# Kernel optimization log

Hardware: AMD Instinct MI355X
Metric: run time of the kernel (lower is better)

## Reference

```python
import jax, jax.numpy as jnp
import numpy as np

NEG_SLOPE = 0.2
EPS = 1e-6


def setup_inputs() -> dict:
    key = jax.random.key(0)
    k1, k2 = jax.random.split(key)
    B, C, N = 4, 64, 32768
    x = jax.random.normal(k1, (B, C, 3, N), dtype=jnp.float32)
    # VNLinear weight: nn.Linear(in, out, bias=False).weight -> [out, in]
    W = jax.random.normal(k2, (C, C), dtype=jnp.float32) * (1.0 / np.sqrt(C))
    return {"x": x, "W": W}


def reference(x, W):
    # VNLinear: kron(W, eye(3)) conv2d == per-3-vector channel mix
    # d[b,o,v,n] = sum_i W[o,i] * x[b,i,v,n]
    d = jnp.einsum('oi,bivn->bovn', W, x)
    dotprod = jnp.sum(x * d, axis=2, keepdims=True)      # [B,C,1,N]
    d_norm_sq = jnp.sum(d * d, axis=2, keepdims=True)    # [B,C,1,N]
    neg = x - (1.0 - NEG_SLOPE) * (dotprod / (d_norm_sq + EPS)) * d
    return jnp.where(dotprod >= 0, x, neg)
```

## Files before the change

### kernel.cpp

```cpp
#include <hip/hip_runtime.h>

#define NEG_SLOPE 0.2f
#define EPS 1e-6f


#define C_CH 64
#define V_DIM 3
#define N_FULL 32768
#define NT 32
#define THREADS 256

typedef __attribute__((ext_vector_type(8))) short bf16x8;
typedef __attribute__((ext_vector_type(4))) float f32x4;

__device__ __forceinline__ ushort f2bf(float f) {
    union { float f; unsigned u; } v; v.f = f;
    unsigned r = v.u + 0x7FFFu + ((v.u >> 16) & 1u);
    return (ushort)(r >> 16);
}
__device__ __forceinline__ float bf2f(ushort s) {
    union { unsigned u; float f; } v; v.u = ((unsigned)s) << 16; return v.f;
}
__device__ __forceinline__ unsigned pack_hl(float x) {
    union { float f; unsigned u; } a; a.f = x;
    unsigned uh = (a.u + 0x8000u) & 0xffff0000u;
    union { unsigned u; float f; } hb; hb.u = uh;
    union { float f; unsigned u; } rb; rb.f = x - hb.f;
    return uh | (rb.u >> 16);
}
__device__ __forceinline__ float u2f(unsigned u) {
    union { unsigned u; float f; } v; v.u = u; return v.f;
}

__global__ void w_split_kernel(const float* __restrict__ W,
                               ushort* __restrict__ whi, ushort* __restrict__ wlo) {
    int i = blockIdx.x * 256 + threadIdx.x;
    if (i < C_CH * C_CH) {
        float w = W[i];
        ushort h = f2bf(w);
        whi[i] = h;
        wlo[i] = f2bf(w - bf2f(h));
    }
}

template<bool USE_WS>
__global__ __launch_bounds__(THREADS, 6)
void vn_mfma32(const float* __restrict__ x,
               const float* __restrict__ Wf,
               const ushort* __restrict__ whi, const ushort* __restrict__ wlo,
               float* __restrict__ out) {
    __shared__ unsigned xs[V_DIM * C_CH][NT];

    const int t    = threadIdx.x;
    const int tile = blockIdx.x;
    const int b    = tile >> 10;
    const int n0   = (tile & 1023) << 5;

    const float* xb = x + (size_t)b * (C_CH * V_DIM * N_FULL) + n0;

    const int lane = t & 63;
    const int w    = t >> 6;
    const int wo   = w >> 1;
    const int wn   = w & 1;
    const int l4   = lane & 15;
    const int hi   = lane >> 4;

    bf16x8 Ah[2][2], Al[2][2];
    if (USE_WS) {
        #pragma unroll
        for (int m = 0; m < 2; ++m)
            #pragma unroll
            for (int kh = 0; kh < 2; ++kh) {
                size_t off = (size_t)(wo * 32 + m * 16 + l4) * C_CH + kh * 32 + hi * 8;
                Ah[m][kh] = *(const bf16x8*)(whi + off);
                Al[m][kh] = *(const bf16x8*)(wlo + off);
            }
    } else {
        #pragma unroll
        for (int m = 0; m < 2; ++m)
            #pragma unroll
            for (int kh = 0; kh < 2; ++kh) {
                const float* wp = Wf + (size_t)(wo * 32 + m * 16 + l4) * C_CH + kh * 32 + hi * 8;
                float4 wa = *(const float4*)wp;
                float4 wb = *(const float4*)(wp + 4);
                float wf[8] = {wa.x, wa.y, wa.z, wa.w, wb.x, wb.y, wb.z, wb.w};
                bf16x8 h, l;
                #pragma unroll
                for (int j = 0; j < 8; ++j) {
                    ushort hb = f2bf(wf[j]);
                    h[j] = (short)hb;
                    l[j] = (short)f2bf(wf[j] - bf2f(hb));
                }
                Ah[m][kh] = h; Al[m][kh] = l;
            }
    }

    #pragma unroll
    for (int it = 0; it < 6; ++it) {
        int idx = t + it * THREADS;
        int r   = idx >> 3;
        int c4  = (idx & 7) << 2;
        int i   = (r * 171) >> 9;
        int v   = r - 3 * i;
        int rowp = v * 64 + i;
        float4 vf4 = *(const float4*)(xb + (size_t)r * N_FULL + c4);
        float vf[4] = {vf4.x, vf4.y, vf4.z, vf4.w};
        unsigned p[4];
        #pragma unroll
        for (int q = 0; q < 4; ++q) p[q] = pack_hl(vf[q]);
        int col = c4 ^ (((rowp >> 3) & 1) << 4);
        *(uint4*)&xs[rowp][col] = *(const uint4*)p;
    }
    __syncthreads();

    f32x4 acc[2][3];
    #pragma unroll
    for (int m = 0; m < 2; ++m)
        #pragma unroll
        for (int v = 0; v < 3; ++v)
            acc[m][v] = (f32x4){0.f, 0.f, 0.f, 0.f};

    const int bcol = (wn * 16 + l4) ^ ((hi & 1) << 4);
    #pragma unroll
    for (int v = 0; v < 3; ++v) {
        #pragma unroll
        for (int kh = 0; kh < 2; ++kh) {
            unsigned p[8];
            #pragma unroll
            for (int j = 0; j < 8; ++j)
                p[j] = xs[v * 64 + kh * 32 + hi * 8 + j][bcol];
            union { bf16x8 v8; unsigned d[4]; } BH, BL;
            #pragma unroll
            for (int q = 0; q < 4; ++q) {
                BH.d[q] = __builtin_amdgcn_perm(p[2 * q + 1], p[2 * q], 0x07060302u);
                BL.d[q] = __builtin_amdgcn_perm(p[2 * q + 1], p[2 * q], 0x05040100u);
            }
            #pragma unroll
            for (int m = 0; m < 2; ++m) {
                acc[m][v] = __builtin_amdgcn_mfma_f32_16x16x32_bf16(Ah[m][kh], BH.v8, acc[m][v], 0, 0, 0);
                acc[m][v] = __builtin_amdgcn_mfma_f32_16x16x32_bf16(Ah[m][kh], BL.v8, acc[m][v], 0, 0, 0);
                acc[m][v] = __builtin_amdgcn_mfma_f32_16x16x32_bf16(Al[m][kh], BH.v8, acc[m][v], 0, 0, 0);
            }
        }
    }

    const int n    = wn * 16 + l4;
    const int ecol = n ^ ((hi >> 1) << 4);
    float* ob = out + (size_t)b * (C_CH * V_DIM * N_FULL) + n0 + n;
    #pragma unroll
    for (int m = 0; m < 2; ++m) {
        #pragma unroll
        for (int r = 0; r < 4; ++r) {
            const int o = wo * 32 + m * 16 + hi * 4 + r;
            float xv[3], dv[3];
            #pragma unroll
            for (int v = 0; v < 3; ++v) {
                unsigned p = xs[v * 64 + o][ecol];
                xv[v] = u2f(p & 0xffff0000u) + u2f(p << 16);
                dv[v] = acc[m][v][r];
            }
            float dot  = xv[0] * dv[0] + xv[1] * dv[1] + xv[2] * dv[2];
            float dnsq = dv[0] * dv[0] + dv[1] * dv[1] + dv[2] * dv[2];
            float f = (1.0f - NEG_SLOPE) * dot / (dnsq + EPS);
            float o0, o1, o2;
            if (dot >= 0.f) {
                o0 = xv[0]; o1 = xv[1]; o2 = xv[2];
            } else {
                o0 = xv[0] - f * dv[0]; o1 = xv[1] - f * dv[1]; o2 = xv[2] - f * dv[2];
            }
            float* op = ob + (size_t)o * (V_DIM * N_FULL);
            op[0 * N_FULL] = o0;
            op[1 * N_FULL] = o1;
            op[2 * N_FULL] = o2;
        }
    }
}

extern "C" void kernel_launch(void* const* d_in, const int* in_sizes, int n_in,
                              void* d_out, int out_size, void* d_ws, size_t ws_size,
                              hipStream_t stream) {
    const float* x = (const float*)d_in[0];
    const float* W = (const float*)d_in[1];
    float* out = (float*)d_out;

    const int B = 4;
    const int blocks = B * (N_FULL / NT);

    if (ws_size >= 2u * C_CH * C_CH * sizeof(ushort)) {
        ushort* whi = (ushort*)d_ws;
        ushort* wlo = whi + C_CH * C_CH;
        w_split_kernel<<<(C_CH * C_CH + 255) / 256, 256, 0, stream>>>(W, whi, wlo);
        vn_mfma32<true><<<blocks, THREADS, 0, stream>>>(x, W, whi, wlo, out);
    } else {
        vn_mfma32<false><<<blocks, THREADS, 0, stream>>>(x, W, nullptr, nullptr, out);
    }
}
```

Baseline: 44.74 us.

## Swap MFMA operands so each lane owns 4 contiguous n for float4 stores

Swaps the A/B operands of the MFMA so x becomes the A operand and W the B operand. Each lane's accumulator then holds 4 consecutive n positions for one output channel instead of 4 channels at one n. The epilogue can read x from LDS as uint4 and write the output as float4, where it used to do scalar loads and stores. The LDS swizzle is extended to keep the new access patterns free of bank conflicts. The change also replaces the division with a fast reciprocal, which slightly alters rounding.

```diff
diff --git a/kernel.cpp b/kernel.cpp
--- a/kernel.cpp
+++ b/kernel.cpp
@@ -23,10 +23,10 @@
 }
 __device__ __forceinline__ unsigned pack_hl(float x) {
     union { float f; unsigned u; } a; a.f = x;
-    unsigned uh = (a.u + 0x8000u) & 0xffff0000u;
-    union { unsigned u; float f; } hb; hb.u = uh;
+    unsigned t0 = a.u + 0x8000u;
+    union { unsigned u; float f; } hb; hb.u = t0 & 0xffff0000u;
     union { float f; unsigned u; } rb; rb.f = x - hb.f;
-    return uh | (rb.u >> 16);
+    return __builtin_amdgcn_perm(t0, rb.u, 0x07060302u);
 }
 __device__ __forceinline__ float u2f(unsigned u) {
     union { unsigned u; float f; } v; v.u = u; return v.f;
@@ -43,6 +43,10 @@
     }
 }
 
+__device__ __forceinline__ int swz(int row) {
+    return ((row & 7) << 2) ^ (((row >> 3) & 1) << 4);
+}
+
 template<bool USE_WS>
 __global__ __launch_bounds__(THREADS, 6)
 void vn_mfma32(const float* __restrict__ x,
@@ -65,15 +69,15 @@
     const int l4   = lane & 15;
     const int hi   = lane >> 4;
 
-    bf16x8 Ah[2][2], Al[2][2];
+    bf16x8 Bh[2][2], Bl[2][2];
     if (USE_WS) {
         #pragma unroll
         for (int m = 0; m < 2; ++m)
             #pragma unroll
             for (int kh = 0; kh < 2; ++kh) {
                 size_t off = (size_t)(wo * 32 + m * 16 + l4) * C_CH + kh * 32 + hi * 8;
-                Ah[m][kh] = *(const bf16x8*)(whi + off);
-                Al[m][kh] = *(const bf16x8*)(wlo + off);
+                Bh[m][kh] = *(const bf16x8*)(whi + off);
+                Bl[m][kh] = *(const bf16x8*)(wlo + off);
             }
     } else {
         #pragma unroll
@@ -91,7 +95,7 @@
                     h[j] = (short)hb;
                     l[j] = (short)f2bf(wf[j] - bf2f(hb));
                 }
-                Ah[m][kh] = h; Al[m][kh] = l;
+                Bh[m][kh] = h; Bl[m][kh] = l;
             }
     }
 
@@ -108,8 +112,7 @@
         unsigned p[4];
         #pragma unroll
         for (int q = 0; q < 4; ++q) p[q] = pack_hl(vf[q]);
-        int col = c4 ^ (((rowp >> 3) & 1) << 4);
-        *(uint4*)&xs[rowp][col] = *(const uint4*)p;
+        *(uint4*)&xs[rowp][c4 ^ swz(rowp)] = *(const uint4*)p;
     }
     __syncthreads();
 
@@ -120,58 +123,64 @@
         for (int v = 0; v < 3; ++v)
             acc[m][v] = (f32x4){0.f, 0.f, 0.f, 0.f};
 
-    const int bcol = (wn * 16 + l4) ^ ((hi & 1) << 4);
+    const int acolb = (wn * 16 + l4) ^ ((hi & 1) << 4);
     #pragma unroll
     for (int v = 0; v < 3; ++v) {
         #pragma unroll
         for (int kh = 0; kh < 2; ++kh) {
+            const int rowb = v * 64 + kh * 32 + hi * 8;
             unsigned p[8];
             #pragma unroll
             for (int j = 0; j < 8; ++j)
-                p[j] = xs[v * 64 + kh * 32 + hi * 8 + j][bcol];
-            union { bf16x8 v8; unsigned d[4]; } BH, BL;
+                p[j] = xs[rowb + j][acolb ^ (j << 2)];
+            union { bf16x8 v8; unsigned d[4]; } AH, AL;
             #pragma unroll
             for (int q = 0; q < 4; ++q) {
-                BH.d[q] = __builtin_amdgcn_perm(p[2 * q + 1], p[2 * q], 0x07060302u);
-                BL.d[q] = __builtin_amdgcn_perm(p[2 * q + 1], p[2 * q], 0x05040100u);
+                AH.d[q] = __builtin_amdgcn_perm(p[2 * q + 1], p[2 * q], 0x07060302u);
+                AL.d[q] = __builtin_amdgcn_perm(p[2 * q + 1], p[2 * q], 0x05040100u);
             }
             #pragma unroll
             for (int m = 0; m < 2; ++m) {
-                acc[m][v] = __builtin_amdgcn_mfma_f32_16x16x32_bf16(Ah[m][kh], BH.v8, acc[m][v], 0, 0, 0);
-                acc[m][v] = __builtin_amdgcn_mfma_f32_16x16x32_bf16(Ah[m][kh], BL.v8, acc[m][v], 0, 0, 0);
-                acc[m][v] = __builtin_amdgcn_mfma_f32_16x16x32_bf16(Al[m][kh], BH.v8, acc[m][v], 0, 0, 0);
-            }
-        }
-    }
-
-    const int n    = wn * 16 + l4;
-    const int ecol = n ^ ((hi >> 1) << 4);
-    float* ob = out + (size_t)b * (C_CH * V_DIM * N_FULL) + n0 + n;
+                acc[m][v] = __builtin_amdgcn_mfma_f32_16x16x32_bf16(AH.v8, Bh[m][kh], acc[m][v], 0, 0, 0);
+                acc[m][v] = __builtin_amdgcn_mfma_f32_16x16x32_bf16(AL.v8, Bh[m][kh], acc[m][v], 0, 0, 0);
+                acc[m][v] = __builtin_amdgcn_mfma_f32_16x16x32_bf16(AH.v8, Bl[m][kh], acc[m][v], 0, 0, 0);
+            }
+        }
+    }
+
+    const int ncol = wn * 16 + hi * 4;
+    const int ecol = ncol ^ ((l4 & 7) << 2) ^ (((l4 >> 3) & 1) << 4);
     #pragma unroll
     for (int m = 0; m < 2; ++m) {
+        const int o = wo * 32 + m * 16 + l4;
+        float xv[3][4];
+        #pragma unroll
+        for (int v = 0; v < 3; ++v) {
+            uint4 p4 = *(const uint4*)&xs[v * 64 + o][ecol];
+            unsigned pw[4] = {p4.x, p4.y, p4.z, p4.w};
+            #pragma unroll
+            for (int q = 0; q < 4; ++q)
+                xv[v][q] = u2f(pw[q] & 0xffff0000u) + u2f(pw[q] << 16);
+        }
+        float fm[4];
         #pragma unroll
         for (int r = 0; r < 4; ++r) {
-            const int o = wo * 32 + m * 16 + hi * 4 + r;
-            float xv[3], dv[3];
-            #pragma unroll
-            for (int v = 0; v < 3; ++v) {
-                unsigned p = xs[v * 64 + o][ecol];
-                xv[v] = u2f(p & 0xffff0000u) + u2f(p << 16);
-                dv[v] = acc[m][v][r];
-            }
-            float dot  = xv[0] * dv[0] + xv[1] * dv[1] + xv[2] * dv[2];
-            float dnsq = dv[0] * dv[0] + dv[1] * dv[1] + dv[2] * dv[2];
-            float f = (1.0f - NEG_SLOPE) * dot / (dnsq + EPS);
-            float o0, o1, o2;
-            if (dot >= 0.f) {
-                o0 = xv[0]; o1 = xv[1]; o2 = xv[2];
-            } else {
-                o0 = xv[0] - f * dv[0]; o1 = xv[1] - f * dv[1]; o2 = xv[2] - f * dv[2];
-            }
-            float* op = ob + (size_t)o * (V_DIM * N_FULL);
-            op[0 * N_FULL] = o0;
-            op[1 * N_FULL] = o1;
-            op[2 * N_FULL] = o2;
+            float d0 = acc[m][0][r], d1 = acc[m][1][r], d2 = acc[m][2][r];
+            float dot  = xv[0][r] * d0 + xv[1][r] * d1 + xv[2][r] * d2;
+            float dnsq = d0 * d0 + d1 * d1 + d2 * d2;
+            float f = (1.0f - NEG_SLOPE) * dot * __builtin_amdgcn_rcpf(dnsq + EPS);
+            fm[r] = (dot >= 0.f) ? 0.f : f;
+        }
+        float* ob = out + (size_t)b * (C_CH * V_DIM * N_FULL)
+                        + (size_t)o * (V_DIM * N_FULL) + n0 + ncol;
+        #pragma unroll
+        for (int v = 0; v < 3; ++v) {
+            float4 o4;
+            o4.x = fmaf(-fm[0], acc[m][v][0], xv[v][0]);
+            o4.y = fmaf(-fm[1], acc[m][v][1], xv[v][1]);
+            o4.z = fmaf(-fm[2], acc[m][v][2], xv[v][2]);
+            o4.w = fmaf(-fm[3], acc[m][v][3], xv[v][3]);
+            *(float4*)(ob + (size_t)v * N_FULL) = o4;
         }
     }
 }
```

Measured after the change: 70.63 us. 1.58x slower.

## Double tile width to 64 columns with 512 threads and cheaper epilogue

Applied to the files above, without the earlier changes.

Each block now covers 64 points of N with 512 threads (8 waves), halving the block count. The LDS swizzle is widened to four 16-column groups to match. The hi/lo bf16 packing now uses a perm instruction, and the epilogue replaces the division and branch with a fast reciprocal and a select feeding FMAs. This is meant to cut per-block overhead and ALU cost, but the doubled LDS tile (48KB) and the launch_bounds of 6 at 512 threads may limit occupancy, and the approximate reciprocal can shift numerics slightly.

```diff
diff --git a/kernel.cpp b/kernel.cpp
--- a/kernel.cpp
+++ b/kernel.cpp
@@ -7,8 +7,8 @@
 #define C_CH 64
 #define V_DIM 3
 #define N_FULL 32768
-#define NT 32
-#define THREADS 256
+#define NT 64
+#define THREADS 512
 
 typedef __attribute__((ext_vector_type(8))) short bf16x8;
 typedef __attribute__((ext_vector_type(4))) float f32x4;
@@ -23,10 +23,10 @@
 }
 __device__ __forceinline__ unsigned pack_hl(float x) {
     union { float f; unsigned u; } a; a.f = x;
-    unsigned uh = (a.u + 0x8000u) & 0xffff0000u;
-    union { unsigned u; float f; } hb; hb.u = uh;
+    unsigned t0 = a.u + 0x8000u;
+    union { unsigned u; float f; } hb; hb.u = t0 & 0xffff0000u;
     union { float f; unsigned u; } rb; rb.f = x - hb.f;
-    return uh | (rb.u >> 16);
+    return __builtin_amdgcn_perm(t0, rb.u, 0x07060302u);
 }
 __device__ __forceinline__ float u2f(unsigned u) {
     union { unsigned u; float f; } v; v.u = u; return v.f;
@@ -43,9 +43,11 @@
     }
 }
 
+__device__ __forceinline__ int swz(int row) { return ((row >> 3) & 3) << 4; }
+
 template<bool USE_WS>
 __global__ __launch_bounds__(THREADS, 6)
-void vn_mfma32(const float* __restrict__ x,
+void vn_mfma64(const float* __restrict__ x,
                const float* __restrict__ Wf,
                const ushort* __restrict__ whi, const ushort* __restrict__ wlo,
                float* __restrict__ out) {
@@ -53,15 +55,15 @@
 
     const int t    = threadIdx.x;
     const int tile = blockIdx.x;
-    const int b    = tile >> 10;
-    const int n0   = (tile & 1023) << 5;
+    const int b    = tile >> 9;
+    const int n0   = (tile & 511) << 6;
 
     const float* xb = x + (size_t)b * (C_CH * V_DIM * N_FULL) + n0;
 
     const int lane = t & 63;
     const int w    = t >> 6;
-    const int wo   = w >> 1;
-    const int wn   = w & 1;
+    const int wo   = w >> 2;
+    const int wn   = w & 3;
     const int l4   = lane & 15;
     const int hi   = lane >> 4;
 
@@ -98,8 +100,8 @@
     #pragma unroll
     for (int it = 0; it < 6; ++it) {
         int idx = t + it * THREADS;
-        int r   = idx >> 3;
-        int c4  = (idx & 7) << 2;
+        int r   = idx >> 4;
+        int c4  = (idx & 15) << 2;
         int i   = (r * 171) >> 9;
         int v   = r - 3 * i;
         int rowp = v * 64 + i;
@@ -108,8 +110,7 @@
         unsigned p[4];
         #pragma unroll
         for (int q = 0; q < 4; ++q) p[q] = pack_hl(vf[q]);
-        int col = c4 ^ (((rowp >> 3) & 1) << 4);
-        *(uint4*)&xs[rowp][col] = *(const uint4*)p;
+        *(uint4*)&xs[rowp][c4 ^ swz(rowp)] = *(const uint4*)p;
     }
     __syncthreads();
 
@@ -120,15 +121,16 @@
         for (int v = 0; v < 3; ++v)
             acc[m][v] = (f32x4){0.f, 0.f, 0.f, 0.f};
 
-    const int bcol = (wn * 16 + l4) ^ ((hi & 1) << 4);
+    const int acol = (wn * 16 + l4) ^ (hi << 4);
     #pragma unroll
     for (int v = 0; v < 3; ++v) {
         #pragma unroll
         for (int kh = 0; kh < 2; ++kh) {
+            const int rowb = v * 64 + kh * 32 + hi * 8;
             unsigned p[8];
             #pragma unroll
             for (int j = 0; j < 8; ++j)
-                p[j] = xs[v * 64 + kh * 32 + hi * 8 + j][bcol];
+                p[j] = xs[rowb + j][acol];
             union { bf16x8 v8; unsigned d[4]; } BH, BL;
             #pragma unroll
             for (int q = 0; q < 4; ++q) {
@@ -144,14 +146,14 @@
         }
     }
 
-    const int n    = wn * 16 + l4;
-    const int ecol = n ^ ((hi >> 1) << 4);
+    const int n = wn * 16 + l4;
     float* ob = out + (size_t)b * (C_CH * V_DIM * N_FULL) + n0 + n;
     #pragma unroll
     for (int m = 0; m < 2; ++m) {
         #pragma unroll
         for (int r = 0; r < 4; ++r) {
             const int o = wo * 32 + m * 16 + hi * 4 + r;
+            const int ecol = n ^ (((m * 2 + (hi >> 1)) & 3) << 4);
             float xv[3], dv[3];
             #pragma unroll
             for (int v = 0; v < 3; ++v) {
@@ -161,13 +163,11 @@
             }
             float dot  = xv[0] * dv[0] + xv[1] * dv[1] + xv[2] * dv[2];
             float dnsq = dv[0] * dv[0] + dv[1] * dv[1] + dv[2] * dv[2];
-            float f = (1.0f - NEG_SLOPE) * dot / (dnsq + EPS);
-            float o0, o1, o2;
-            if (dot >= 0.f) {
-                o0 = xv[0]; o1 = xv[1]; o2 = xv[2];
-            } else {
-                o0 = xv[0] - f * dv[0]; o1 = xv[1] - f * dv[1]; o2 = xv[2] - f * dv[2];
-            }
+            float f = (1.0f - NEG_SLOPE) * dot * __builtin_amdgcn_rcpf(dnsq + EPS);
+            f = (dot >= 0.f) ? 0.f : f;
+            float o0 = fmaf(-f, dv[0], xv[0]);
+            float o1 = fmaf(-f, dv[1], xv[1]);
+            float o2 = fmaf(-f, dv[2], xv[2]);
             float* op = ob + (size_t)o * (V_DIM * N_FULL);
             op[0 * N_FULL] = o0;
             op[1 * N_FULL] = o1;
@@ -190,8 +190,8 @@
         ushort* whi = (ushort*)d_ws;
         ushort* wlo = whi + C_CH * C_CH;
         w_split_kernel<<<(C_CH * C_CH + 255) / 256, 256, 0, stream>>>(W, whi, wlo);
-        vn_mfma32<true><<<blocks, THREADS, 0, stream>>>(x, W, whi, wlo, out);
+        vn_mfma64<true><<<blocks, THREADS, 0, stream>>>(x, W, whi, wlo, out);
     } else {
-        vn_mfma32<false><<<blocks, THREADS, 0, stream>>>(x, W, nullptr, nullptr, out);
+        vn_mfma64<false><<<blocks, THREADS, 0, stream>>>(x, W, nullptr, nullptr, out);
     }
 }
```

New measurement: 43.60 us. 2.6% less time.
